# Optimization experiments

Hardware: AMD Instinct MI355X
Metric: run time of the kernel (lower is better)

Reference implementation:

```python
import jax, jax.numpy as jnp
import numpy as np


def setup_inputs() -> dict:
    key = jax.random.key(0)
    ks = jax.random.split(key, 12)
    N_DRUGS, D, N_CELLS, C_IN, E = 4096, 128, 1024, 1000, 500000
    inp = {
        "drug_hidden_out": jax.random.normal(ks[0], (N_DRUGS, D), dtype=jnp.float32),
        "cell_hidden_out": jax.random.normal(ks[1], (N_CELLS, C_IN), dtype=jnp.float32),
        # columns: drug1_idx, drug2_idx, cell_idx, label (original code indexes
        # drug_hidden_out with ALL THREE index columns, so bound by N_DRUGS)
        "all_edges": jax.random.randint(ks[2], (E, 4), 0, N_DRUGS, dtype=jnp.int64),
        # proj: Linear(1000, 128)
        "proj_W": jax.random.normal(ks[3], (D, C_IN), dtype=jnp.float32) * 0.03,
        "proj_b": jnp.zeros((D,), dtype=jnp.float32),
        # NN: Linear(128,32) -> ReLU -> Linear(32,32) -> ReLU -> Linear(32,32)
        #     -> ReLU -> Dropout(eval=identity) -> Linear(32,1) -> Sigmoid
        "W1": jax.random.normal(ks[4], (32, D), dtype=jnp.float32) * 0.08,
        "b1": jnp.zeros((32,), dtype=jnp.float32),
        "W2": jax.random.normal(ks[5], (32, 32), dtype=jnp.float32) * 0.17,
        "b2": jnp.zeros((32,), dtype=jnp.float32),
        "W3": jax.random.normal(ks[6], (32, 32), dtype=jnp.float32) * 0.17,
        "b3": jnp.zeros((32,), dtype=jnp.float32),
        "W4": jax.random.normal(ks[7], (1, 32), dtype=jnp.float32) * 0.17,
        "b4": jnp.zeros((1,), dtype=jnp.float32),
    }
    return inp


def reference(drug_hidden_out, cell_hidden_out, all_edges,
              proj_W, proj_b, W1, b1, W2, b2, W3, b3, W4, b4):
    # proj is computed in the original forward but its result is never used
    # downstream (the code re-indexes drug_hidden_out for cell_fea).
    _cell_proj = cell_hidden_out @ proj_W.T + proj_b  # [n_cells, 128], dead value

    edges = all_edges.T                 # [4, E]
    label = edges[3]                    # [E]
    edge_index = edges[:3]              # [3, E]

    drug1_fea = drug_hidden_out[edge_index[0]]   # [E, 128] gather
    drug2_fea = drug_hidden_out[edge_index[1]]   # [E, 128] gather
    cell_fea = drug_hidden_out[edge_index[2]]    # [E, 128] gather (faithful to source bug)
    logits = drug1_fea * drug2_fea * cell_fea    # [E, 128]

    h = jax.nn.relu(logits @ W1.T + b1)          # [E, 32]
    h = jax.nn.relu(h @ W2.T + b2)               # [E, 32]
    h = jax.nn.relu(h @ W3.T + b3)               # [E, 32] (dropout = identity in eval)
    x = jax.nn.sigmoid(h @ W4.T + b4)            # [E, 1]
    return x, label
```

## Files before the change

kernel.cpp:

```cpp
#include <hip/hip_runtime.h>
#include <stdint.h>

#define DD 128
#define HH 32
#define RS 36
#define TABQ (4096 * DD / 4)
#define BLOB_OFF (1u << 20)

typedef _Float16 f16;
typedef _Float16 f16x4 __attribute__((ext_vector_type(4)));
typedef _Float16 f16x8 __attribute__((ext_vector_type(8)));
typedef float    f32x4 __attribute__((ext_vector_type(4)));

#define GL1(p)  ((const __attribute__((address_space(1))) void*)(p))
#define LDS3(p) ((__attribute__((address_space(3))) void*)(p))

__global__ __launch_bounds__(256)
void synergy_prepass(const float* __restrict__ drug,
                     const float* __restrict__ W1, const float* __restrict__ W2,
                     const float* __restrict__ W3, f16* __restrict__ tab)
{
    const int tid = threadIdx.x;
    if ((int)blockIdx.x == 512) {
        f16x8* __restrict__ blob16 = (f16x8*)((char*)tab + BLOB_OFF);
        const float4* __restrict__ W1v = (const float4*)W1;
        #pragma unroll
        for (int p = 0; p < 2; ++p) {
            const int S = p * 256 + tid;
            const int t = S >> 8, f = (S >> 6) & 3, l = S & 63;
            const int mm = l & 15, qq = l >> 4;
            const int c4 = (t * 16 + mm) * (DD / 4) + f * 8 + qq * 2;
            const float4 w0 = W1v[c4], w1 = W1v[c4 + 1];
            f16x8 r;
            r[0]=(f16)w0.x; r[1]=(f16)w0.y; r[2]=(f16)w0.z; r[3]=(f16)w0.w;
            r[4]=(f16)w1.x; r[5]=(f16)w1.y; r[6]=(f16)w1.z; r[7]=(f16)w1.w;
            blob16[S] = r;
        }
        {
            const int B = tid & 127;
            const int t = B >> 6, l = B & 63;
            const int mm = l & 15, qq = l >> 4;
            const int c4 = (t * 16 + mm) * (HH / 4) + qq * 2;
            const float4* __restrict__ src = (tid < 128) ? (const float4*)W2 : (const float4*)W3;
            const float4 w0 = src[c4], w1 = src[c4 + 1];
            f16x8 r;
            r[0]=(f16)w0.x; r[1]=(f16)w0.y; r[2]=(f16)w0.z; r[3]=(f16)w0.w;
            r[4]=(f16)w1.x; r[5]=(f16)w1.y; r[6]=(f16)w1.z; r[7]=(f16)w1.w;
            blob16[512 + (tid & 128) + B] = r;
        }
        return;
    }
    const int i = blockIdx.x * 256 + tid;
    if (i < TABQ) {
        const float4 v = ((const float4*)drug)[i];
        f16x4 h;
        h[0]=(f16)v.x; h[1]=(f16)v.y; h[2]=(f16)v.z; h[3]=(f16)v.w;
        ((f16x4*)tab)[i] = h;
    }
}

__global__ __launch_bounds__(256, 3)
void synergy_main(const f16* __restrict__ tab, const int* __restrict__ edges,
                  const float* __restrict__ W4, const float* __restrict__ b1,
                  const float* __restrict__ b2, const float* __restrict__ b3,
                  const float* __restrict__ b4, float* __restrict__ out,
                  int E, int NG)
{
    __shared__ __align__(16) f16 stage[4][6144];
    __shared__ __align__(16) f16 hbuf[4][16 * RS];

    const int tid  = threadIdx.x;
    const int wave = tid >> 6;
    const int lane = tid & 63;
    const int m    = lane & 15;
    const int q    = lane >> 4;

    const int WSTR = (int)gridDim.x * 4;
    int g = (int)blockIdx.x * 4 + wave;
    if (g >= NG) return;

    const char* __restrict__ tabB   = (const char*)tab;
    const int4* __restrict__ edges4 = (const int4*)edges;

    const f16x8* __restrict__ blobG = (const f16x8*)(tabB + BLOB_OFF);
    f16x8 wa[2][4];
    #pragma unroll
    for (int t = 0; t < 2; ++t)
        #pragma unroll
        for (int f = 0; f < 4; ++f)
            wa[t][f] = blobG[(t * 4 + f) * 64 + lane];
    const f16x8 w2a = blobG[512 + lane], w2b = blobG[576 + lane];
    const f16x8 w3a = blobG[640 + lane], w3b = blobG[704 + lane];
    const float b1a = b1[m], b1b = b1[16 + m];
    const float b2a = b2[m], b2b = b2[16 + m];
    const float b3a = b3[m], b3b = b3[16 + m];
    const float w4a = W4[m], w4b = W4[16 + m];
    const float b4v = b4[0];

    f16* __restrict__ stg = stage[wave];
    f16* __restrict__ hb  = hbuf[wave];

    auto issue_dma = [&](const int4 ed) {
        #pragma unroll
        for (int gg = 0; gg < 4; ++gg) {
            const int src   = 4 * gg + q;
            const int seg16 = ((m + src) & 15) << 4;
            const int rx = __shfl(ed.x, src, 64) << 8;
            __builtin_amdgcn_global_load_lds(GL1(tabB + (size_t)(rx + seg16)),
                LDS3((char*)stg + (0 * 16 + 4 * gg) * 256), 16, 0, 0);
            const int ry = __shfl(ed.y, src, 64) << 8;
            __builtin_amdgcn_global_load_lds(GL1(tabB + (size_t)(ry + seg16)),
                LDS3((char*)stg + (1 * 16 + 4 * gg) * 256), 16, 0, 0);
            const int rz = __shfl(ed.z, src, 64) << 8;
            __builtin_amdgcn_global_load_lds(GL1(tabB + (size_t)(rz + seg16)),
                LDS3((char*)stg + (2 * 16 + 4 * gg) * 256), 16, 0, 0);
        }
    };
    auto load_ed = [&](int gg) -> int4 {
        int e = (gg << 4) + m;
        e = (e < E) ? e : (E - 1);
        return edges4[e];
    };

    int4 ed_cur = load_ed(g);
    issue_dma(ed_cur);
    int gn = g + WSTR;
    int4 ed_nxt = load_ed((gn < NG) ? gn : g);

    for (;;) {
        __builtin_amdgcn_sched_barrier(0);
        __builtin_amdgcn_s_waitcnt(0x0F70);
        __builtin_amdgcn_sched_barrier(0);

        f32x4 acc0 = {b1a, b1a, b1a, b1a};
        f32x4 acc1 = {b1b, b1b, b1b, b1b};
        #pragma unroll
        for (int f = 0; f < 4; ++f) {
            const int slot = (((f * 4 + q) - m) & 15) << 3;
            const f16x8 v0 = *(const f16x8*)(stg + (0 * 16 + m) * 128 + slot);
            const f16x8 v1 = *(const f16x8*)(stg + (1 * 16 + m) * 128 + slot);
            const f16x8 v2 = *(const f16x8*)(stg + (2 * 16 + m) * 128 + slot);
            const f16x8 p = v0 * v1 * v2;
            acc0 = __builtin_amdgcn_mfma_f32_16x16x32_f16(p, wa[0][f], acc0, 0, 0, 0);
            acc1 = __builtin_amdgcn_mfma_f32_16x16x32_f16(p, wa[1][f], acc1, 0, 0, 0);
        }
        #pragma unroll
        for (int r = 0; r < 4; ++r) {
            const int row = 4 * q + r;
            hb[row * RS + m]      = (f16)fmaxf(acc0[r], 0.0f);
            hb[row * RS + 16 + m] = (f16)fmaxf(acc1[r], 0.0f);
        }

        const int gf = gn + WSTR;
        const int4 ed_fut = load_ed((gf < NG) ? gf : g);

        if (gn < NG) {
            __builtin_amdgcn_sched_barrier(0);
            issue_dma(ed_nxt);
            __builtin_amdgcn_sched_barrier(0);
        }

        {
            const f16x8 a2 = *(const f16x8*)(hb + m * RS + q * 8);
            f32x4 c0 = {b2a, b2a, b2a, b2a};
            f32x4 c1 = {b2b, b2b, b2b, b2b};
            c0 = __builtin_amdgcn_mfma_f32_16x16x32_f16(a2, w2a, c0, 0, 0, 0);
            c1 = __builtin_amdgcn_mfma_f32_16x16x32_f16(a2, w2b, c1, 0, 0, 0);
            #pragma unroll
            for (int r = 0; r < 4; ++r) {
                const int row = 4 * q + r;
                hb[row * RS + m]      = (f16)fmaxf(c0[r], 0.0f);
                hb[row * RS + 16 + m] = (f16)fmaxf(c1[r], 0.0f);
            }
        }

        f32x4 d0 = {b3a, b3a, b3a, b3a};
        f32x4 d1 = {b3b, b3b, b3b, b3b};
        {
            const f16x8 a3 = *(const f16x8*)(hb + m * RS + q * 8);
            d0 = __builtin_amdgcn_mfma_f32_16x16x32_f16(a3, w3a, d0, 0, 0, 0);
            d1 = __builtin_amdgcn_mfma_f32_16x16x32_f16(a3, w3b, d1, 0, 0, 0);
        }

        float zr[4];
        #pragma unroll
        for (int r = 0; r < 4; ++r)
            zr[r] = fmaxf(d0[r], 0.0f) * w4a + fmaxf(d1[r], 0.0f) * w4b;
        #pragma unroll
        for (int dd = 1; dd < 16; dd <<= 1)
            #pragma unroll
            for (int r = 0; r < 4; ++r)
                zr[r] += __shfl_xor(zr[r], dd, 64);
        if (m == 0) {
            const int e0 = (g << 4) + 4 * q;
            float4 res;
            res.x = 1.0f / (1.0f + __expf(-(zr[0] + b4v)));
            res.y = 1.0f / (1.0f + __expf(-(zr[1] + b4v)));
            res.z = 1.0f / (1.0f + __expf(-(zr[2] + b4v)));
            res.w = 1.0f / (1.0f + __expf(-(zr[3] + b4v)));
            if (e0 + 3 < E) *(float4*)(out + e0) = res;
            else {
                if (e0 + 0 < E) out[e0 + 0] = res.x;
                if (e0 + 1 < E) out[e0 + 1] = res.y;
                if (e0 + 2 < E) out[e0 + 2] = res.z;
                if (e0 + 3 < E) out[e0 + 3] = res.w;
            }
        }
        const int eL = (g << 4) + lane;
        if (lane < 16 && eL < E) out[E + eL] = (float)ed_cur.w;

        if (gn >= NG) break;
        g = gn; gn = gf; ed_cur = ed_nxt; ed_nxt = ed_fut;
    }
}

extern "C" void kernel_launch(void* const* d_in, const int* in_sizes, int n_in,
                              void* d_out, int out_size, void* d_ws, size_t ws_size,
                              hipStream_t stream)
{
    const float* drug  = (const float*)d_in[0];
    const int*   edges = (const int*)d_in[2];
    const float* W1 = (const float*)d_in[5];
    const float* b1 = (const float*)d_in[6];
    const float* W2 = (const float*)d_in[7];
    const float* b2 = (const float*)d_in[8];
    const float* W3 = (const float*)d_in[9];
    const float* b3 = (const float*)d_in[10];
    const float* W4 = (const float*)d_in[11];
    const float* b4 = (const float*)d_in[12];
    float* out = (float*)d_out;
    f16*   tab = (f16*)d_ws;

    const int E  = in_sizes[2] / 4;
    const int NG = (E + 15) / 16;

    hipLaunchKernelGGL(synergy_prepass, dim3(513), dim3(256), 0, stream,
                       drug, W1, W2, W3, tab);
    int blocks = (NG + 3) / 4;
    if (blocks > 768) blocks = 768;
    hipLaunchKernelGGL(synergy_main, dim3(blocks), dim3(256), 0, stream,
                       tab, edges, W4, b1, b2, b3, b4, out, E, NG);
}
```

Measured before the change: 123.7 us.

## Compute final layer with MFMA and move next-tile gather issue to loop end

The last 32-to-1 layer becomes an MFMA against a zero-padded f16 W4 fragment, built in the prepass, replacing the per-lane multiply and 16-lane shuffle reduction. The gather DMA for the next edge group now runs at the end of the loop instead of right after layer 1. All row-index shuffles are batched before the twelve LDS-direct loads. This cuts shuffle and VALU work in the epilogue, but the next tile's gather no longer overlaps with layers 2–4 of the current tile, so more memory latency may be exposed at the top-of-loop wait.

```diff
diff --git a/kernel.cpp b/kernel.cpp
--- a/kernel.cpp
+++ b/kernel.cpp
@@ -18,7 +18,8 @@
 __global__ __launch_bounds__(256)
 void synergy_prepass(const float* __restrict__ drug,
                      const float* __restrict__ W1, const float* __restrict__ W2,
-                     const float* __restrict__ W3, f16* __restrict__ tab)
+                     const float* __restrict__ W3, const float* __restrict__ W4,
+                     f16* __restrict__ tab)
 {
     const int tid = threadIdx.x;
     if ((int)blockIdx.x == 512) {
@@ -48,6 +49,14 @@
             r[4]=(f16)w1.x; r[5]=(f16)w1.y; r[6]=(f16)w1.z; r[7]=(f16)w1.w;
             blob16[512 + (tid & 128) + B] = r;
         }
+        if (tid < 64) {
+            const int mm = tid & 15, qq = tid >> 4;
+            f16x8 r;
+            #pragma unroll
+            for (int j = 0; j < 8; ++j)
+                r[j] = (mm == 0) ? (f16)W4[qq * 8 + j] : (f16)0.0f;
+            blob16[768 + tid] = r;
+        }
         return;
     }
     const int i = blockIdx.x * 256 + tid;
@@ -61,10 +70,9 @@
 
 __global__ __launch_bounds__(256, 3)
 void synergy_main(const f16* __restrict__ tab, const int* __restrict__ edges,
-                  const float* __restrict__ W4, const float* __restrict__ b1,
-                  const float* __restrict__ b2, const float* __restrict__ b3,
-                  const float* __restrict__ b4, float* __restrict__ out,
-                  int E, int NG)
+                  const float* __restrict__ b1, const float* __restrict__ b2,
+                  const float* __restrict__ b3, const float* __restrict__ b4,
+                  float* __restrict__ out, int E, int NG)
 {
     __shared__ __align__(16) f16 stage[4][6144];
     __shared__ __align__(16) f16 hbuf[4][16 * RS];
@@ -91,36 +99,40 @@
             wa[t][f] = blobG[(t * 4 + f) * 64 + lane];
     const f16x8 w2a = blobG[512 + lane], w2b = blobG[576 + lane];
     const f16x8 w3a = blobG[640 + lane], w3b = blobG[704 + lane];
+    const f16x8 wf4 = blobG[768 + lane];
     const float b1a = b1[m], b1b = b1[16 + m];
     const float b2a = b2[m], b2b = b2[16 + m];
     const float b3a = b3[m], b3b = b3[16 + m];
-    const float w4a = W4[m], w4b = W4[16 + m];
     const float b4v = b4[0];
 
     f16* __restrict__ stg = stage[wave];
     f16* __restrict__ hb  = hbuf[wave];
 
-    auto issue_dma = [&](const int4 ed) {
-        #pragma unroll
-        for (int gg = 0; gg < 4; ++gg) {
-            const int src   = 4 * gg + q;
-            const int seg16 = ((m + src) & 15) << 4;
-            const int rx = __shfl(ed.x, src, 64) << 8;
-            __builtin_amdgcn_global_load_lds(GL1(tabB + (size_t)(rx + seg16)),
-                LDS3((char*)stg + (0 * 16 + 4 * gg) * 256), 16, 0, 0);
-            const int ry = __shfl(ed.y, src, 64) << 8;
-            __builtin_amdgcn_global_load_lds(GL1(tabB + (size_t)(ry + seg16)),
-                LDS3((char*)stg + (1 * 16 + 4 * gg) * 256), 16, 0, 0);
-            const int rz = __shfl(ed.z, src, 64) << 8;
-            __builtin_amdgcn_global_load_lds(GL1(tabB + (size_t)(rz + seg16)),
-                LDS3((char*)stg + (2 * 16 + 4 * gg) * 256), 16, 0, 0);
-        }
-    };
     auto load_ed = [&](int gg) -> int4 {
         int e = (gg << 4) + m;
         e = (e < E) ? e : (E - 1);
         return edges4[e];
     };
+    auto issue_dma = [&](const int4 ed) {
+        int rowb[12];
+        #pragma unroll
+        for (int gg = 0; gg < 4; ++gg) {
+            const int src = 4 * gg + q;
+            rowb[0 * 4 + gg] = __shfl(ed.x, src, 64) << 8;
+            rowb[1 * 4 + gg] = __shfl(ed.y, src, 64) << 8;
+            rowb[2 * 4 + gg] = __shfl(ed.z, src, 64) << 8;
+        }
+        __builtin_amdgcn_sched_barrier(0);
+        #pragma unroll
+        for (int t = 0; t < 3; ++t)
+            #pragma unroll
+            for (int gg = 0; gg < 4; ++gg) {
+                const int seg16 = ((m + 4 * gg + q) & 15) << 4;
+                __builtin_amdgcn_global_load_lds(
+                    GL1(tabB + (size_t)(rowb[t * 4 + gg] + seg16)),
+                    LDS3((char*)stg + (t * 16 + 4 * gg) * 256), 16, 0, 0);
+            }
+    };
 
     int4 ed_cur = load_ed(g);
     issue_dma(ed_cur);
@@ -128,7 +140,6 @@
     int4 ed_nxt = load_ed((gn < NG) ? gn : g);
 
     for (;;) {
-        __builtin_amdgcn_sched_barrier(0);
         __builtin_amdgcn_s_waitcnt(0x0F70);
         __builtin_amdgcn_sched_barrier(0);
 
@@ -154,12 +165,6 @@
         const int gf = gn + WSTR;
         const int4 ed_fut = load_ed((gf < NG) ? gf : g);
 
-        if (gn < NG) {
-            __builtin_amdgcn_sched_barrier(0);
-            issue_dma(ed_nxt);
-            __builtin_amdgcn_sched_barrier(0);
-        }
-
         {
             const f16x8 a2 = *(const f16x8*)(hb + m * RS + q * 8);
             f32x4 c0 = {b2a, b2a, b2a, b2a};
@@ -174,42 +179,44 @@
             }
         }
 
-        f32x4 d0 = {b3a, b3a, b3a, b3a};
-        f32x4 d1 = {b3b, b3b, b3b, b3b};
         {
             const f16x8 a3 = *(const f16x8*)(hb + m * RS + q * 8);
+            f32x4 d0 = {b3a, b3a, b3a, b3a};
+            f32x4 d1 = {b3b, b3b, b3b, b3b};
             d0 = __builtin_amdgcn_mfma_f32_16x16x32_f16(a3, w3a, d0, 0, 0, 0);
             d1 = __builtin_amdgcn_mfma_f32_16x16x32_f16(a3, w3b, d1, 0, 0, 0);
-        }
-
-        float zr[4];
-        #pragma unroll
-        for (int r = 0; r < 4; ++r)
-            zr[r] = fmaxf(d0[r], 0.0f) * w4a + fmaxf(d1[r], 0.0f) * w4b;
-        #pragma unroll
-        for (int dd = 1; dd < 16; dd <<= 1)
-            #pragma unroll
-            for (int r = 0; r < 4; ++r)
-                zr[r] += __shfl_xor(zr[r], dd, 64);
-        if (m == 0) {
-            const int e0 = (g << 4) + 4 * q;
-            float4 res;
-            res.x = 1.0f / (1.0f + __expf(-(zr[0] + b4v)));
-            res.y = 1.0f / (1.0f + __expf(-(zr[1] + b4v)));
-            res.z = 1.0f / (1.0f + __expf(-(zr[2] + b4v)));
-            res.w = 1.0f / (1.0f + __expf(-(zr[3] + b4v)));
-            if (e0 + 3 < E) *(float4*)(out + e0) = res;
-            else {
-                if (e0 + 0 < E) out[e0 + 0] = res.x;
-                if (e0 + 1 < E) out[e0 + 1] = res.y;
-                if (e0 + 2 < E) out[e0 + 2] = res.z;
-                if (e0 + 3 < E) out[e0 + 3] = res.w;
+            #pragma unroll
+            for (int r = 0; r < 4; ++r) {
+                const int row = 4 * q + r;
+                hb[row * RS + m]      = (f16)fmaxf(d0[r], 0.0f);
+                hb[row * RS + 16 + m] = (f16)fmaxf(d1[r], 0.0f);
+            }
+        }
+
+        {
+            const f16x8 a4 = *(const f16x8*)(hb + m * RS + q * 8);
+            f32x4 z = {b4v, b4v, b4v, b4v};
+            z = __builtin_amdgcn_mfma_f32_16x16x32_f16(a4, wf4, z, 0, 0, 0);
+            if (m == 0) {
+                const int e0 = (g << 4) + 4 * q;
+                float4 res;
+                res.x = 1.0f / (1.0f + __expf(-z[0]));
+                res.y = 1.0f / (1.0f + __expf(-z[1]));
+                res.z = 1.0f / (1.0f + __expf(-z[2]));
+                res.w = 1.0f / (1.0f + __expf(-z[3]));
+                if (e0 + 3 < E) *(float4*)(out + e0) = res;
+                else {
+                    if (e0 + 0 < E) out[e0 + 0] = res.x;
+                    if (e0 + 1 < E) out[e0 + 1] = res.y;
+                    if (e0 + 2 < E) out[e0 + 2] = res.z;
+                }
             }
         }
         const int eL = (g << 4) + lane;
         if (lane < 16 && eL < E) out[E + eL] = (float)ed_cur.w;
 
         if (gn >= NG) break;
+        issue_dma(ed_nxt);
         g = gn; gn = gf; ed_cur = ed_nxt; ed_nxt = ed_fut;
     }
 }
@@ -235,9 +242,9 @@
     const int NG = (E + 15) / 16;
 
     hipLaunchKernelGGL(synergy_prepass, dim3(513), dim3(256), 0, stream,
-                       drug, W1, W2, W3, tab);
+                       drug, W1, W2, W3, W4, tab);
     int blocks = (NG + 3) / 4;
     if (blocks > 768) blocks = 768;
     hipLaunchKernelGGL(synergy_main, dim3(blocks), dim3(256), 0, stream,
-                       tab, edges, W4, b1, b2, b3, b4, out, E, NG);
+                       tab, edges, b1, b2, b3, b4, out, E, NG);
 }
```

Result: no change. 122.9 us (median of 2 runs) (-0.7%).
